# Kernel tuning notes

Hardware: AMD Instinct MI355X
Metric: run time of the kernel (lower is better)

Reference implementation:

```python
import jax, jax.numpy as jnp
import numpy as np

B, T, E, H = 32, 577, 1024, 16
D = E // H  # head_dim = 64

def setup_inputs() -> dict:
    key = jax.random.key(0)
    ks = jax.random.split(key, 5)
    s = 1.0 / np.sqrt(E)
    return {
        "x": jax.random.normal(ks[0], (B, T, E), dtype=jnp.float32),
        "Wq": jax.random.normal(ks[1], (E, E), dtype=jnp.float32) * s,
        "bq": jnp.zeros((E,), dtype=jnp.float32),
        "Wk": jax.random.normal(ks[2], (E, E), dtype=jnp.float32) * s,
        "bk": jnp.zeros((E,), dtype=jnp.float32),
        "Wv": jax.random.normal(ks[3], (E, E), dtype=jnp.float32) * s,
        "bv": jnp.zeros((E,), dtype=jnp.float32),
        "Wo": jax.random.normal(ks[4], (E, E), dtype=jnp.float32) * s,
        "bo": jnp.zeros((E,), dtype=jnp.float32),
    }

def reference(x, Wq, bq, Wk, bk, Wv, bv, Wo, bo):
    # Linear projections (torch Linear: x @ W.T + b; here W stored as [in,out])
    q = (x @ Wq + bq).reshape(B, T, H, D).transpose(0, 2, 1, 3)  # [B,H,T,D]
    k = (x @ Wk + bk).reshape(B, T, H, D).transpose(0, 2, 1, 3)
    v = (x @ Wv + bv).reshape(B, T, H, D).transpose(0, 2, 1, 3)
    scores = jnp.einsum('bhqd,bhkd->bhqk', q, k) / jnp.sqrt(jnp.float32(D))
    att = jax.nn.softmax(scores, axis=-1)  # dropout is identity in eval
    out = jnp.einsum('bhqk,bhkd->bhqd', att, v)
    out = out.transpose(0, 2, 1, 3).reshape(B, T, E)
    return out @ Wo + bo
```

## Files before the change

### kernel.cpp

```cpp
#include <hip/hip_runtime.h>
#include <cmath>

#define BDIM 32
#define TDIM 577
#define TPAD 640
#define EDIM 1024
#define HDIM 16
#define DDIM 64
#define MDIM (BDIM * TDIM)
#define MTILES 145
#define MPAD (MTILES * 128)
#define MT256 73
#define NTILES_K 16

typedef unsigned short u16;
typedef __bf16 bf16x8 __attribute__((ext_vector_type(8)));
typedef float f32x4 __attribute__((ext_vector_type(4)));
typedef u16 u16x8 __attribute__((ext_vector_type(8)));

__device__ __forceinline__ u16 f2bf(float f) {
    unsigned int u = __float_as_uint(f);
    u = (u + 0x7FFFu + ((u >> 16) & 1u)) >> 16;
    return (u16)u;
}

__device__ __forceinline__ void gload_lds16(const void* g, void* l) {
    __builtin_amdgcn_global_load_lds(
        (const __attribute__((address_space(1))) unsigned int*)g,
        (__attribute__((address_space(3))) unsigned int*)l, 16, 0, 0);
}

#define SB()  __builtin_amdgcn_sched_barrier(0)
#define BAR() __builtin_amdgcn_s_barrier()
#define WAIT_LGKM0() asm volatile("s_waitcnt lgkmcnt(0)" ::: "memory")


__global__ __launch_bounds__(256) void cast_x(const float* __restrict__ x,
                                              u16* __restrict__ o, int nelem)
{
    int i = (blockIdx.x * 256 + threadIdx.x) * 8;
    if (i >= nelem) return;
    float4 a = *(const float4*)(x + i);
    float4 b = *(const float4*)(x + i + 4);
    u16x8 r;
    r[0] = f2bf(a.x); r[1] = f2bf(a.y); r[2] = f2bf(a.z); r[3] = f2bf(a.w);
    r[4] = f2bf(b.x); r[5] = f2bf(b.y); r[6] = f2bf(b.z); r[7] = f2bf(b.w);
    *(u16x8*)(o + i) = r;
}

__global__ __launch_bounds__(256) void cast_wt(
    const float* __restrict__ W0, const float* __restrict__ W1,
    const float* __restrict__ W2, const float* __restrict__ W3,
    u16* __restrict__ T0, u16* __restrict__ T1,
    u16* __restrict__ T2, u16* __restrict__ T3)
{
    __shared__ float tile[32][33];
    const int z = blockIdx.z;
    const float* __restrict__ W = (z == 0) ? W0 : (z == 1) ? W1 : (z == 2) ? W2 : W3;
    u16* __restrict__ T = (z == 0) ? T0 : (z == 1) ? T1 : (z == 2) ? T2 : T3;
    const int bn = blockIdx.x * 32;
    const int bk = blockIdx.y * 32;
    const int tx = threadIdx.x & 31, ty = threadIdx.x >> 5;
#pragma unroll
    for (int p = 0; p < 4; ++p) {
        int k = bk + p * 8 + ty;
        tile[p * 8 + ty][tx] = W[(size_t)k * EDIM + bn + tx];
    }
    __syncthreads();
#pragma unroll
    for (int p = 0; p < 4; ++p) {
        int n = bn + p * 8 + ty;
        T[(size_t)n * EDIM + bk + tx] = f2bf(tile[tx][p * 8 + ty]);
    }
}

__global__ __launch_bounds__(512, 2) void gemm256(
    const u16* __restrict__ A,
    const u16* __restrict__ W0, const u16* __restrict__ W1, const u16* __restrict__ W2,
    const float* __restrict__ b0, const float* __restrict__ b1, const float* __restrict__ b2,
    void* __restrict__ o0, void* __restrict__ o1, void* __restrict__ o2,
    int mode)
{
    __shared__ u16 lds[2][2][2][8192];

    const int z = blockIdx.z;
    const u16* __restrict__ Wt     = (z == 0) ? W0 : ((z == 1) ? W1 : W2);
    const float* __restrict__ bias = (z == 0) ? b0 : ((z == 1) ? b1 : b2);
    void* __restrict__ dst         = (z == 0) ? o0 : ((z == 1) ? o1 : o2);

    const int tid   = threadIdx.x;
    const int wave  = tid >> 6;
    const int lane  = tid & 63;
    const int mlane = lane & 15;
    const int quad  = lane >> 4;
    const int wm = wave >> 2;
    const int wn = wave & 3;
    const int sq8 = (quad ^ ((mlane >> 1) & 3)) * 8;

    const int loc = blockIdx.y * gridDim.x + blockIdx.x;
    const int cc = loc & 7, cp = loc >> 3;
    const int work = (cc < 4 ? cc * 37 : 148 + (cc - 4) * 36) + cp;
    const int n0 = (work & 3) * 256;
    const int m0 = (work >> 2) * 256;

    f32x4 acc[8][4];
#pragma unroll
    for (int i = 0; i < 8; ++i)
#pragma unroll
        for (int j = 0; j < 4; ++j) acc[i][j] = (f32x4)(0.f);

    auto stage = [&](int db, int mat, int hf, int t) {
        if (t >= NTILES_K) return;
        const u16* src = (mat == 0) ? (A  + (size_t)(m0 + hf * 128) * EDIM)
                                    : (Wt + (size_t)(n0 + hf * 128) * EDIM);
        const int kb = t * 64;
#pragma unroll
        for (int r = 0; r < 2; ++r) {
            int c = r * 512 + tid;
            int ks = c >> 9, row = (c >> 2) & 127, j4 = c & 3;
            int js = j4 ^ ((row >> 1) & 3);
            gload_lds16(src + (size_t)row * EDIM + kb + ks * 32 + js * 8,
                        &lds[db][mat][hf][(r * 512 + wave * 64) * 8]);
        }
    };

    const int arow = wm * 64 + mlane;
    const int brow = (wn & 1) * 64 + mlane;
    const int bhf  = wn >> 1;
    bf16x8 bq[4][2];

#define GPHASE(RB, QI, STAGE_STMT)                                             \
    do {                                                                       \
        const u16* la = &lds[cb][0][RB][0];                                    \
        bf16x8 af[2][2];                                                       \
        _Pragma("unroll") for (int ri2 = 0; ri2 < 2; ++ri2)                    \
            _Pragma("unroll") for (int ks = 0; ks < 2; ++ks)                   \
                af[ri2][ks] = *(const bf16x8*)&la[ks * 4096 +                  \
                    (arow + ((QI) * 2 + ri2) * 16) * 32 + sq8];                \
        STAGE_STMT;                                                            \
        SB(); BAR(); WAIT_LGKM0(); SB();                                       \
        __builtin_amdgcn_s_setprio(1);                                         \
        _Pragma("unroll") for (int ri2 = 0; ri2 < 2; ++ri2)                    \
            _Pragma("unroll") for (int j = 0; j < 4; ++j)                      \
                _Pragma("unroll") for (int ks = 0; ks < 2; ++ks)               \
                    acc[(RB) * 4 + (QI) * 2 + ri2][j] =                        \
                        __builtin_amdgcn_mfma_f32_16x16x32_bf16(               \
                            af[ri2][ks], bq[j][ks],                            \
                            acc[(RB) * 4 + (QI) * 2 + ri2][j], 0, 0, 0);       \
        __builtin_amdgcn_s_setprio(0);                                         \
    } while (0)

    stage(0, 0, 0, 0);
    stage(0, 1, 0, 0);
    stage(0, 1, 1, 0);
    stage(0, 0, 1, 0);
    stage(1, 1, 0, 1);
    stage(1, 1, 1, 1);
    stage(1, 0, 0, 1);
    asm volatile("s_waitcnt vmcnt(6)" ::: "memory");
    SB(); BAR();

    for (int t = 0; t < NTILES_K; ++t) {
        const int cb = t & 1;
        const int nb = cb ^ 1;

        {
            const u16* lb = &lds[cb][1][bhf][0];
#pragma unroll
            for (int j = 0; j < 4; ++j)
#pragma unroll
                for (int ks = 0; ks < 2; ++ks)
                    bq[j][ks] = *(const bf16x8*)&lb[ks * 4096 +
                        (brow + j * 16) * 32 + sq8];
        }
        GPHASE(0, 0, stage(nb, 0, 1, t + 1));
        SB(); BAR();
        GPHASE(0, 1, stage(cb, 1, 0, t + 2));
        SB(); BAR();
        GPHASE(1, 0, stage(cb, 1, 1, t + 2));
        SB(); BAR();
        GPHASE(1, 1, stage(cb, 0, 0, t + 2));
        if (t < NTILES_K - 1) {
            if (t == NTILES_K - 2) { asm volatile("s_waitcnt vmcnt(0)" ::: "memory"); }
            else                   { asm volatile("s_waitcnt vmcnt(6)" ::: "memory"); }
            SB(); BAR();
        }
    }
#undef GPHASE

#pragma unroll
    for (int j = 0; j < 4; ++j) {
        int n = n0 + wn * 64 + j * 16 + mlane;
        float bv = bias[n];
        if (mode == 1) {
            float* df = (float*)dst;
#pragma unroll
            for (int mr = 0; mr < 8; ++mr) {
                int mb = m0 + wm * 64 + (mr >> 2) * 128 + (mr & 3) * 16 + quad * 4;
#pragma unroll
                for (int r = 0; r < 4; ++r) {
                    int gm = mb + r;
                    if (gm < MDIM) df[(size_t)gm * EDIM + n] = acc[mr][j][r] + bv;
                }
            }
        } else {
            u16* db = (u16*)dst;
            int h = n >> 6, d = n & 63;
#pragma unroll
            for (int mr = 0; mr < 8; ++mr) {
                int mb = m0 + wm * 64 + (mr >> 2) * 128 + (mr & 3) * 16 + quad * 4;
#pragma unroll
                for (int r = 0; r < 4; ++r) {
                    int gm = mb + r;
                    if (gm < MDIM) {
                        int b = gm / TDIM, t = gm - b * TDIM;
                        u16 val = f2bf(acc[mr][j][r] + bv);
                        if (z == 2)
                            db[((size_t)(b * HDIM + h) * DDIM + d) * TPAD + t] = val;
                        else
                            db[((size_t)(b * HDIM + h) * TPAD + t) * DDIM + d] = val;
                    }
                }
            }
        }
    }
}

__global__ __launch_bounds__(256) void attn_mfma(
    const u16* __restrict__ qg, const u16* __restrict__ kg,
    const u16* __restrict__ vtg, u16* __restrict__ outg)
{
    __shared__ u16 Qs[4096];
    __shared__ u16 Ks[4096];
    __shared__ u16 Vts[4096];
    __shared__ u16 Ps[4608];

    const int tid = threadIdx.x;
    const int wave = tid >> 6;
    const int lane = tid & 63;
    const int ml = lane & 15;
    const int quad = lane >> 4;
    const int sq8 = (quad ^ ((ml >> 1) & 3)) * 8;
    const int h = blockIdx.y, b = blockIdx.z;
    const int q0 = blockIdx.x * 64;
    const u16* qb = qg + ((size_t)b * HDIM + h) * TPAD * DDIM;
    const u16* kb = kg + ((size_t)b * HDIM + h) * TPAD * DDIM;
    const u16* vb = vtg + ((size_t)b * HDIM + h) * DDIM * TPAD;

#pragma unroll
    for (int r = 0; r < 2; ++r) {
        int c = r * 256 + tid;
        int row = (c >> 2) & 63, kc = c >> 8, d8 = c & 3;
        int js = d8 ^ ((row >> 1) & 3);
        gload_lds16(qb + (size_t)(q0 + row) * DDIM + kc * 32 + js * 8,
                    &Qs[(r * 256 + wave * 64) * 8]);
    }
    __syncthreads();

    bf16x8 aq0 = *(const bf16x8*)&Qs[(wave * 16 + ml) * 32 + sq8];
    bf16x8 aq1 = *(const bf16x8*)&Qs[2048 + (wave * 16 + ml) * 32 + sq8];

    f32x4 oacc[4];
#pragma unroll
    for (int dt = 0; dt < 4; ++dt) oacc[dt] = (f32x4)(0.f);
    float m_i[4], l_i[4];
#pragma unroll
    for (int r = 0; r < 4; ++r) { m_i[r] = -INFINITY; l_i[r] = 0.f; }

    for (int kv0 = 0; kv0 < TDIM; kv0 += 64) {
        __syncthreads();
#pragma unroll
        for (int r = 0; r < 2; ++r) {
            int c = r * 256 + tid;
            int row = (c >> 2) & 63, kc = c >> 8, d8 = c & 3;
            int js = d8 ^ ((row >> 1) & 3);
            gload_lds16(kb + (size_t)(kv0 + row) * DDIM + kc * 32 + js * 8,
                        &Ks[(r * 256 + wave * 64) * 8]);
            gload_lds16(vb + (size_t)row * TPAD + kv0 + kc * 32 + js * 8,
                        &Vts[(r * 256 + wave * 64) * 8]);
        }
        __syncthreads();

        f32x4 sacc[4];
#pragma unroll
        for (int jt = 0; jt < 4; ++jt) {
            bf16x8 bk0 = *(const bf16x8*)&Ks[(jt * 16 + ml) * 32 + sq8];
            bf16x8 bk1 = *(const bf16x8*)&Ks[2048 + (jt * 16 + ml) * 32 + sq8];
            f32x4 sa = (f32x4)(0.f);
            sa = __builtin_amdgcn_mfma_f32_16x16x32_bf16(aq0, bk0, sa, 0, 0, 0);
            sa = __builtin_amdgcn_mfma_f32_16x16x32_bf16(aq1, bk1, sa, 0, 0, 0);
            sacc[jt] = sa;
        }

        float p[4][4];
#pragma unroll
        for (int r = 0; r < 4; ++r) {
            float cm = -INFINITY;
#pragma unroll
            for (int jt = 0; jt < 4; ++jt) {
                bool valid = (kv0 + jt * 16 + ml) < TDIM;
                float sv = valid ? sacc[jt][r] * 0.125f : -INFINITY;
                p[jt][r] = sv;
                cm = fmaxf(cm, sv);
            }
            cm = fmaxf(cm, __shfl_xor(cm, 1, 64));
            cm = fmaxf(cm, __shfl_xor(cm, 2, 64));
            cm = fmaxf(cm, __shfl_xor(cm, 4, 64));
            cm = fmaxf(cm, __shfl_xor(cm, 8, 64));
            float mn = fmaxf(m_i[r], cm);
            float alpha = __expf(m_i[r] - mn);
            float rs = 0.f;
#pragma unroll
            for (int jt = 0; jt < 4; ++jt) {
                float e = __expf(p[jt][r] - mn);
                p[jt][r] = e;
                rs += e;
            }
            rs += __shfl_xor(rs, 1, 64);
            rs += __shfl_xor(rs, 2, 64);
            rs += __shfl_xor(rs, 4, 64);
            rs += __shfl_xor(rs, 8, 64);
            l_i[r] = l_i[r] * alpha + rs;
            m_i[r] = mn;
#pragma unroll
            for (int dt = 0; dt < 4; ++dt) oacc[dt][r] *= alpha;
        }

#pragma unroll
        for (int jt = 0; jt < 4; ++jt)
#pragma unroll
            for (int r = 0; r < 4; ++r)
                Ps[wave * 1152 + (jt >> 1) * 576 + (quad * 4 + r) * 36 + (jt & 1) * 16 + ml]
                    = f2bf(p[jt][r]);
        __syncthreads();

        bf16x8 pf0 = *(const bf16x8*)&Ps[wave * 1152 + ml * 36 + quad * 8];
        bf16x8 pf1 = *(const bf16x8*)&Ps[wave * 1152 + 576 + ml * 36 + quad * 8];

#pragma unroll
        for (int dt = 0; dt < 4; ++dt) {
            bf16x8 bv0 = *(const bf16x8*)&Vts[(dt * 16 + ml) * 32 + sq8];
            bf16x8 bv1 = *(const bf16x8*)&Vts[2048 + (dt * 16 + ml) * 32 + sq8];
            oacc[dt] = __builtin_amdgcn_mfma_f32_16x16x32_bf16(pf0, bv0, oacc[dt], 0, 0, 0);
            oacc[dt] = __builtin_amdgcn_mfma_f32_16x16x32_bf16(pf1, bv1, oacc[dt], 0, 0, 0);
        }
    }

#pragma unroll
    for (int r = 0; r < 4; ++r) {
        int t = q0 + wave * 16 + quad * 4 + r;
        if (t >= TDIM) continue;
        float inv = 1.f / l_i[r];
        size_t rowoff = ((size_t)b * TDIM + t) * EDIM + h * DDIM;
#pragma unroll
        for (int dt = 0; dt < 4; ++dt)
            outg[rowoff + dt * 16 + ml] = f2bf(oacc[dt][r] * inv);
    }
}

extern "C" void kernel_launch(void* const* d_in, const int* in_sizes, int n_in,
                              void* d_out, int out_size, void* d_ws, size_t ws_size,
                              hipStream_t stream)
{
    const float* x  = (const float*)d_in[0];
    const float* Wq = (const float*)d_in[1];
    const float* bq = (const float*)d_in[2];
    const float* Wk = (const float*)d_in[3];
    const float* bk = (const float*)d_in[4];
    const float* Wv = (const float*)d_in[5];
    const float* bv = (const float*)d_in[6];
    const float* Wo = (const float*)d_in[7];
    const float* bo = (const float*)d_in[8];
    float* out = (float*)d_out;

    const size_t hsz = (size_t)BDIM * HDIM * TPAD * DDIM;
    u16* qb  = (u16*)d_ws;
    u16* kb  = qb + hsz;
    u16* vtb = kb + hsz;
    u16* xb  = vtb + hsz;
    u16* abb = xb;
    u16* wtq = xb + (size_t)MPAD * EDIM;
    u16* wtk = wtq + (size_t)EDIM * EDIM;
    u16* wtv = wtk + (size_t)EDIM * EDIM;
    u16* wto = wtv + (size_t)EDIM * EDIM;

    cast_x<<<(MDIM * EDIM / 8 + 255) / 256, 256, 0, stream>>>(x, xb, MDIM * EDIM);
    cast_wt<<<dim3(32, 32, 4), 256, 0, stream>>>(Wq, Wk, Wv, Wo, wtq, wtk, wtv, wto);

    gemm256<<<dim3(EDIM / 256, MT256, 3), 512, 0, stream>>>(
        xb, wtq, wtk, wtv, bq, bk, bv, (void*)qb, (void*)kb, (void*)vtb, 0);

    attn_mfma<<<dim3(TPAD / 64, HDIM, BDIM), 256, 0, stream>>>(qb, kb, vtb, abb);

    gemm256<<<dim3(EDIM / 256, MT256, 1), 512, 0, stream>>>(
        abb, wto, wto, wto, bo, bo, bo, (void*)out, (void*)out, (void*)out, 1);
}
```

Baseline: 630.4 us.

## Prefetch A fragments one phase ahead with partial LDS waits and fewer barriers

Restructures the GEMM main loop so LDS reads of the A fragments for the next phase are issued into a second register set before the current phase's MFMAs. It uses lgkmcnt(4) partial waits instead of full drains and removes one barrier per phase. The per-thread global-load addressing for staging is also hoisted out of the loop. The goal is to hide LDS latency and cut synchronisation stalls, at the cost of extra VGPRs and tighter correctness constraints on buffer reuse.

```diff
diff --git a/kernel.cpp b/kernel.cpp
--- a/kernel.cpp
+++ b/kernel.cpp
@@ -33,6 +33,7 @@
 #define SB()  __builtin_amdgcn_sched_barrier(0)
 #define BAR() __builtin_amdgcn_s_barrier()
 #define WAIT_LGKM0() asm volatile("s_waitcnt lgkmcnt(0)" ::: "memory")
+#define WAIT_LGKM4() asm volatile("s_waitcnt lgkmcnt(4)" ::: "memory")
 
 
 __global__ __launch_bounds__(256) void cast_x(const float* __restrict__ x,
@@ -109,46 +110,48 @@
 #pragma unroll
         for (int j = 0; j < 4; ++j) acc[i][j] = (f32x4)(0.f);
 
+    int srow[2], soff[2], ldso[2];
+#pragma unroll
+    for (int r = 0; r < 2; ++r) {
+        int c = r * 512 + tid;
+        int ks = c >> 9, row = (c >> 2) & 127, j4 = c & 3;
+        int js = j4 ^ ((row >> 1) & 3);
+        srow[r] = row;
+        soff[r] = ks * 32 + js * 8;
+        ldso[r] = (r * 512 + wave * 64) * 8;
+    }
     auto stage = [&](int db, int mat, int hf, int t) {
         if (t >= NTILES_K) return;
         const u16* src = (mat == 0) ? (A  + (size_t)(m0 + hf * 128) * EDIM)
                                     : (Wt + (size_t)(n0 + hf * 128) * EDIM);
         const int kb = t * 64;
 #pragma unroll
-        for (int r = 0; r < 2; ++r) {
-            int c = r * 512 + tid;
-            int ks = c >> 9, row = (c >> 2) & 127, j4 = c & 3;
-            int js = j4 ^ ((row >> 1) & 3);
-            gload_lds16(src + (size_t)row * EDIM + kb + ks * 32 + js * 8,
-                        &lds[db][mat][hf][(r * 512 + wave * 64) * 8]);
-        }
+        for (int r = 0; r < 2; ++r)
+            gload_lds16(src + (size_t)srow[r] * EDIM + kb + soff[r],
+                        &lds[db][mat][hf][ldso[r]]);
     };
 
     const int arow = wm * 64 + mlane;
     const int brow = (wn & 1) * 64 + mlane;
     const int bhf  = wn >> 1;
-    bf16x8 bq[4][2];
-
-#define GPHASE(RB, QI, STAGE_STMT)                                             \
-    do {                                                                       \
-        const u16* la = &lds[cb][0][RB][0];                                    \
-        bf16x8 af[2][2];                                                       \
-        _Pragma("unroll") for (int ri2 = 0; ri2 < 2; ++ri2)                    \
-            _Pragma("unroll") for (int ks = 0; ks < 2; ++ks)                   \
-                af[ri2][ks] = *(const bf16x8*)&la[ks * 4096 +                  \
-                    (arow + ((QI) * 2 + ri2) * 16) * 32 + sq8];                \
-        STAGE_STMT;                                                            \
-        SB(); BAR(); WAIT_LGKM0(); SB();                                       \
-        __builtin_amdgcn_s_setprio(1);                                         \
+    bf16x8 bq[4][2], afA[2][2], afB[2][2];
+
+#define READ_A(dstf, RB, QI)                                                   \
+    _Pragma("unroll") for (int ri2 = 0; ri2 < 2; ++ri2)                        \
+        _Pragma("unroll") for (int ks = 0; ks < 2; ++ks)                       \
+            dstf[ri2][ks] = *(const bf16x8*)&lds[cb][0][RB][ks * 4096 +        \
+                (arow + ((QI) * 2 + ri2) * 16) * 32 + sq8];
+
+#define MFMA16(RB, QI, f)                                                      \
+    __builtin_amdgcn_s_setprio(1);                                             \
+    _Pragma("unroll") for (int ks = 0; ks < 2; ++ks)                           \
         _Pragma("unroll") for (int ri2 = 0; ri2 < 2; ++ri2)                    \
             _Pragma("unroll") for (int j = 0; j < 4; ++j)                      \
-                _Pragma("unroll") for (int ks = 0; ks < 2; ++ks)               \
-                    acc[(RB) * 4 + (QI) * 2 + ri2][j] =                        \
-                        __builtin_amdgcn_mfma_f32_16x16x32_bf16(               \
-                            af[ri2][ks], bq[j][ks],                            \
-                            acc[(RB) * 4 + (QI) * 2 + ri2][j], 0, 0, 0);       \
-        __builtin_amdgcn_s_setprio(0);                                         \
-    } while (0)
+                acc[(RB) * 4 + (QI) * 2 + ri2][j] =                            \
+                    __builtin_amdgcn_mfma_f32_16x16x32_bf16(                   \
+                        f[ri2][ks], bq[j][ks],                                 \
+                        acc[(RB) * 4 + (QI) * 2 + ri2][j], 0, 0, 0);           \
+    __builtin_amdgcn_s_setprio(0);
 
     stage(0, 0, 0, 0);
     stage(0, 1, 0, 0);
@@ -158,7 +161,7 @@
     stage(1, 1, 1, 1);
     stage(1, 0, 0, 1);
     asm volatile("s_waitcnt vmcnt(6)" ::: "memory");
-    SB(); BAR();
+    SB(); BAR(); SB();
 
     for (int t = 0; t < NTILES_K; ++t) {
         const int cb = t & 1;
@@ -173,20 +176,33 @@
                     bq[j][ks] = *(const bf16x8*)&lb[ks * 4096 +
                         (brow + j * 16) * 32 + sq8];
         }
-        GPHASE(0, 0, stage(nb, 0, 1, t + 1));
-        SB(); BAR();
-        GPHASE(0, 1, stage(cb, 1, 0, t + 2));
-        SB(); BAR();
-        GPHASE(1, 0, stage(cb, 1, 1, t + 2));
-        SB(); BAR();
-        GPHASE(1, 1, stage(cb, 0, 0, t + 2));
+        READ_A(afA, 0, 0);
+        READ_A(afB, 0, 1);
+        stage(nb, 0, 1, t + 1);
+        SB(); WAIT_LGKM4(); SB();
+        MFMA16(0, 0, afA);
+        BAR(); SB();
+        READ_A(afA, 1, 0);
+        stage(cb, 1, 0, t + 2);
+        SB(); WAIT_LGKM4(); SB();
+        MFMA16(0, 1, afB);
+        BAR(); SB();
+        READ_A(afB, 1, 1);
+        stage(cb, 1, 1, t + 2);
+        SB(); WAIT_LGKM4(); SB();
+        MFMA16(1, 0, afA);
+        BAR(); SB();
+        stage(cb, 0, 0, t + 2);
+        SB(); WAIT_LGKM0(); SB();
+        MFMA16(1, 1, afB);
         if (t < NTILES_K - 1) {
             if (t == NTILES_K - 2) { asm volatile("s_waitcnt vmcnt(0)" ::: "memory"); }
             else                   { asm volatile("s_waitcnt vmcnt(6)" ::: "memory"); }
-            SB(); BAR();
-        }
-    }
-#undef GPHASE
+            SB(); BAR(); SB();
+        }
+    }
+#undef READ_A
+#undef MFMA16
 
 #pragma unroll
     for (int j = 0; j < 4; ++j) {
```

Result: faster. 608.6 us (-3.5%).

## Replace direct-to-LDS GEMM staging with register-staged double buffering

Applied to the files above, without the earlier changes.

The projection GEMM main loop stops using global_load_lds async copies with fine-grained phased barriers. It now loads the next K-tile into registers, writes them into the other LDS buffer after compute, and keeps one barrier per iteration. The A fragments are read in two halves, each followed by a larger batch of MFMAs. This cuts the number of barriers and sync points, at the cost of many more VGPRs for staging, and the full vmcnt(0) wait before each LDS write may expose global memory latency.

```diff
diff --git a/kernel.cpp b/kernel.cpp
--- a/kernel.cpp
+++ b/kernel.cpp
@@ -33,7 +33,7 @@
 #define SB()  __builtin_amdgcn_sched_barrier(0)
 #define BAR() __builtin_amdgcn_s_barrier()
 #define WAIT_LGKM0() asm volatile("s_waitcnt lgkmcnt(0)" ::: "memory")
-
+#define WAIT_VM0()   asm volatile("s_waitcnt vmcnt(0)" ::: "memory")
 
 __global__ __launch_bounds__(256) void cast_x(const float* __restrict__ x,
                                               u16* __restrict__ o, int nelem)
@@ -109,84 +109,93 @@
 #pragma unroll
         for (int j = 0; j < 4; ++j) acc[i][j] = (f32x4)(0.f);
 
-    auto stage = [&](int db, int mat, int hf, int t) {
-        if (t >= NTILES_K) return;
-        const u16* src = (mat == 0) ? (A  + (size_t)(m0 + hf * 128) * EDIM)
-                                    : (Wt + (size_t)(n0 + hf * 128) * EDIM);
-        const int kb = t * 64;
-#pragma unroll
-        for (int r = 0; r < 2; ++r) {
-            int c = r * 512 + tid;
-            int ks = c >> 9, row = (c >> 2) & 127, j4 = c & 3;
-            int js = j4 ^ ((row >> 1) & 3);
-            gload_lds16(src + (size_t)row * EDIM + kb + ks * 32 + js * 8,
-                        &lds[db][mat][hf][(r * 512 + wave * 64) * 8]);
-        }
-    };
+    const u16* gp[8];
+    int ldso[8];
+#pragma unroll
+    for (int i = 0; i < 8; ++i) {
+        int c = ((i & 1) ? 512 : 0) + tid;
+        int ks = c >> 9, row = (c >> 2) & 127, j4 = c & 3;
+        int mat = i >> 2, half = (i >> 1) & 1;
+        const u16* base = mat ? (Wt + (size_t)(n0 + half * 128) * EDIM)
+                              : (A  + (size_t)(m0 + half * 128) * EDIM);
+        gp[i] = base + (size_t)row * EDIM + ks * 32 + j4 * 8;
+        ldso[i] = ks * 4096 + row * 32 + (j4 ^ ((row >> 1) & 3)) * 8;
+    }
+
+    u16x8 stg[8];
+#define LOAD8(T)                                                               \
+    _Pragma("unroll") for (int i = 0; i < 8; ++i)                              \
+        stg[i] = *(const u16x8*)(gp[i] + (T) * 64);
+#define WRITE8(DB)                                                             \
+    _Pragma("unroll") for (int i = 0; i < 8; ++i)                              \
+        *(u16x8*)&lds[DB][i >> 2][(i >> 1) & 1][ldso[i]] = stg[i];
 
     const int arow = wm * 64 + mlane;
     const int brow = (wn & 1) * 64 + mlane;
     const int bhf  = wn >> 1;
-    bf16x8 bq[4][2];
-
-#define GPHASE(RB, QI, STAGE_STMT)                                             \
-    do {                                                                       \
-        const u16* la = &lds[cb][0][RB][0];                                    \
-        bf16x8 af[2][2];                                                       \
-        _Pragma("unroll") for (int ri2 = 0; ri2 < 2; ++ri2)                    \
-            _Pragma("unroll") for (int ks = 0; ks < 2; ++ks)                   \
-                af[ri2][ks] = *(const bf16x8*)&la[ks * 4096 +                  \
-                    (arow + ((QI) * 2 + ri2) * 16) * 32 + sq8];                \
-        STAGE_STMT;                                                            \
-        SB(); BAR(); WAIT_LGKM0(); SB();                                       \
-        __builtin_amdgcn_s_setprio(1);                                         \
-        _Pragma("unroll") for (int ri2 = 0; ri2 < 2; ++ri2)                    \
-            _Pragma("unroll") for (int j = 0; j < 4; ++j)                      \
-                _Pragma("unroll") for (int ks = 0; ks < 2; ++ks)               \
-                    acc[(RB) * 4 + (QI) * 2 + ri2][j] =                        \
-                        __builtin_amdgcn_mfma_f32_16x16x32_bf16(               \
-                            af[ri2][ks], bq[j][ks],                            \
-                            acc[(RB) * 4 + (QI) * 2 + ri2][j], 0, 0, 0);       \
-        __builtin_amdgcn_s_setprio(0);                                         \
-    } while (0)
-
-    stage(0, 0, 0, 0);
-    stage(0, 1, 0, 0);
-    stage(0, 1, 1, 0);
-    stage(0, 0, 1, 0);
-    stage(1, 1, 0, 1);
-    stage(1, 1, 1, 1);
-    stage(1, 0, 0, 1);
-    asm volatile("s_waitcnt vmcnt(6)" ::: "memory");
-    SB(); BAR();
+
+    LOAD8(0);
+    WAIT_VM0(); SB();
+    WRITE8(0);
+    LOAD8(1);
+    WAIT_LGKM0(); SB();
+    BAR(); SB();
 
     for (int t = 0; t < NTILES_K; ++t) {
         const int cb = t & 1;
-        const int nb = cb ^ 1;
-
-        {
-            const u16* lb = &lds[cb][1][bhf][0];
-#pragma unroll
-            for (int j = 0; j < 4; ++j)
-#pragma unroll
-                for (int ks = 0; ks < 2; ++ks)
-                    bq[j][ks] = *(const bf16x8*)&lb[ks * 4096 +
-                        (brow + j * 16) * 32 + sq8];
-        }
-        GPHASE(0, 0, stage(nb, 0, 1, t + 1));
-        SB(); BAR();
-        GPHASE(0, 1, stage(cb, 1, 0, t + 2));
-        SB(); BAR();
-        GPHASE(1, 0, stage(cb, 1, 1, t + 2));
-        SB(); BAR();
-        GPHASE(1, 1, stage(cb, 0, 0, t + 2));
+        const u16* lb  = &lds[cb][1][bhf][0];
+        const u16* la0 = &lds[cb][0][0][0];
+        const u16* la1 = &lds[cb][0][1][0];
+
+        bf16x8 bq[4][2], af[4][2];
+#pragma unroll
+        for (int j = 0; j < 4; ++j)
+#pragma unroll
+            for (int ks = 0; ks < 2; ++ks)
+                bq[j][ks] = *(const bf16x8*)&lb[ks * 4096 + (brow + j * 16) * 32 + sq8];
+#pragma unroll
+        for (int rr = 0; rr < 4; ++rr)
+#pragma unroll
+            for (int ks = 0; ks < 2; ++ks)
+                af[rr][ks] = *(const bf16x8*)&la0[ks * 4096 + (arow + rr * 16) * 32 + sq8];
+        WAIT_LGKM0(); SB();
+        __builtin_amdgcn_s_setprio(1);
+#pragma unroll
+        for (int ks = 0; ks < 2; ++ks)
+#pragma unroll
+            for (int rr = 0; rr < 4; ++rr)
+#pragma unroll
+                for (int j = 0; j < 4; ++j)
+                    acc[rr][j] = __builtin_amdgcn_mfma_f32_16x16x32_bf16(
+                        af[rr][ks], bq[j][ks], acc[rr][j], 0, 0, 0);
+        __builtin_amdgcn_s_setprio(0);
+#pragma unroll
+        for (int rr = 0; rr < 4; ++rr)
+#pragma unroll
+            for (int ks = 0; ks < 2; ++ks)
+                af[rr][ks] = *(const bf16x8*)&la1[ks * 4096 + (arow + rr * 16) * 32 + sq8];
+        WAIT_LGKM0(); SB();
+        __builtin_amdgcn_s_setprio(1);
+#pragma unroll
+        for (int ks = 0; ks < 2; ++ks)
+#pragma unroll
+            for (int rr = 0; rr < 4; ++rr)
+#pragma unroll
+                for (int j = 0; j < 4; ++j)
+                    acc[4 + rr][j] = __builtin_amdgcn_mfma_f32_16x16x32_bf16(
+                        af[rr][ks], bq[j][ks], acc[4 + rr][j], 0, 0, 0);
+        __builtin_amdgcn_s_setprio(0);
+
         if (t < NTILES_K - 1) {
-            if (t == NTILES_K - 2) { asm volatile("s_waitcnt vmcnt(0)" ::: "memory"); }
-            else                   { asm volatile("s_waitcnt vmcnt(6)" ::: "memory"); }
-            SB(); BAR();
-        }
-    }
-#undef GPHASE
+            WAIT_VM0(); SB();
+            WRITE8(cb ^ 1);
+            if (t < NTILES_K - 2) LOAD8(t + 2);
+            WAIT_LGKM0(); SB();
+            BAR(); SB();
+        }
+    }
+#undef LOAD8
+#undef WRITE8
 
 #pragma unroll
     for (int j = 0; j < 4; ++j) {
```

After: 629.2 us. About the same (-0.2%).
